# Optimization experiments

Hardware: AMD Instinct MI355X
Metric: run time of the kernel (lower is better)

The kernel has to match this reference:

```python
import jax, jax.numpy as jnp
import numpy as np

N = 100000   # nodes (users+objects merged into one table)
M = 32768    # interactions (edges)
D = 256      # emb_dim == inter_dim
E = 2        # etypes: trusts, rates


def setup_inputs() -> dict:
    key = jax.random.key(0)
    ks = jax.random.split(key, 24)
    s = 1.0 / np.sqrt(D)
    f = lambda k, shp: (jax.random.normal(k, shp, dtype=jnp.float32) * s)
    return {
        "src": jax.random.randint(ks[0], (M,), 0, N),
        "dst": jax.random.randint(ks[1], (M,), 0, N),
        "etype": jax.random.randint(ks[2], (M,), 0, E),
        "dt": jax.random.uniform(ks[3], (M,), dtype=jnp.float32),
        "hid": f(ks[4], (N, D)),
        "cell": f(ks[5], (N, D)),
        # per-etype relation MLPs (source side and target side), layer==1 -> Lin-ReLU-Lin
        "W1s": f(ks[6], (E, D, D)), "b1s": f(ks[7], (E, D)),
        "W2s": f(ks[8], (E, D, D)), "b2s": f(ks[9], (E, D)),
        "W1g": f(ks[10], (E, D, D)), "b1g": f(ks[11], (E, D)),
        "W2g": f(ks[12], (E, D, D)), "b2g": f(ks[13], (E, D)),
        # attention combine (p, q, linear_s, linear_g)
        "p_w": f(ks[14], (D,)), "p_b": jnp.zeros((), jnp.float32),
        "q_w": f(ks[15], (D,)), "q_b": jnp.zeros((), jnp.float32),
        "Ws_w": f(ks[16], (D, D)), "Ws_b": f(ks[17], (D,)),
        "Wg_w": f(ks[18], (D, D)), "Wg_b": f(ks[19], (D,)),
        # time-aware LSTM cell (TLSTMCell(inter_dim=D, emb_dim=D))
        "Wx": f(ks[20], (D, 4 * D)), "Wh": f(ks[21], (D, 4 * D)),
        "b_lstm": jnp.zeros((4 * D,), jnp.float32),
        # final score head
        "w_out": f(ks[22], (D,)), "b_out": jnp.zeros((), jnp.float32),
        "decay_w": jnp.float32(0.1),
    }


def _rel_mlp(x, W1, b1, W2, b2, onehot):
    # x: [M,D]; W1,W2: [E,D,D]; dispatch through per-etype MLP, select by etype.
    h = jax.nn.relu(jnp.einsum('md,edk->emk', x, W1) + b1[:, None, :])   # [E,M,D]
    y = jnp.einsum('emd,edk->emk', h, W2) + b2[:, None, :]               # [E,M,D]
    return jnp.einsum('emd,me->md', y, onehot)                            # [M,D]


def reference(src, dst, etype, dt, hid, cell,
              W1s, b1s, W2s, b2s, W1g, b1g, W2g, b2g,
              p_w, p_b, q_w, q_b, Ws_w, Ws_b, Wg_w, Wg_b,
              Wx, Wh, b_lstm, w_out, b_out, decay_w):
    onehot = jax.nn.one_hot(etype, E, dtype=hid.dtype)  # [M,E]
    h_s = hid[src]   # [M,D] source hidden
    h_g = hid[dst]   # [M,D] target hidden
    c_g = cell[dst]  # [M,D] target cell

    # relation-specific MLPs (RelationNN)
    msg_s = _rel_mlp(h_s, W1s, b1s, W2s, b2s, onehot)
    msg_g = _rel_mlp(h_g, W1g, b1g, W2g, b2g, onehot)

    # attention-gated interaction combine (p/q + linear_s/linear_g)
    a = jax.nn.sigmoid(msg_s @ p_w + p_b + msg_g @ q_w + q_b)[:, None]  # [M,1]
    x = a * (msg_s @ Ws_w.T + Ws_b) + (1.0 - a) * (msg_g @ Wg_w.T + Wg_b)

    # time decay of target cell state (Decay, exp method)
    c_dec = c_g * jnp.exp(-jnp.abs(decay_w) * dt)[:, None]

    # TLSTM cell update for target node
    gates = x @ Wx + h_g @ Wh + b_lstm                                    # [M,4D]
    i_g, f_g, g_g, o_g = jnp.split(gates, 4, axis=-1)
    c_new = jax.nn.sigmoid(f_g) * c_dec + jax.nn.sigmoid(i_g) * jnp.tanh(g_g)
    h_new = jax.nn.sigmoid(o_g) * jnp.tanh(c_new)

    # edge score head (linear -> sigmoid)
    score = jax.nn.sigmoid(h_new @ w_out + b_out)                         # [M]
    return score, h_new, c_new
```

## Files before the change

kernel.cpp:

```cpp
#include <hip/hip_runtime.h>


#define M_EDGES 32768
#define S_TOP   32896
#define TROWS   64
#define GRID_MEGA (S_TOP / TROWS)

typedef __bf16 bf16_t;
typedef __bf16 bf16x8 __attribute__((ext_vector_type(8)));
typedef float  f32x4  __attribute__((ext_vector_type(4)));

#define OFF_W1ST 0
#define OFF_W2ST 131072
#define OFF_W1GT 262144
#define OFF_W2GT 393216
#define OFF_WST  524288
#define OFF_WGT  589824
#define OFF_WXT  655360
#define OFF_WHT  917504
#define WBUF_ELEMS 1179648

__device__ __forceinline__ float sigm_f(float x) { return 1.f / (1.f + __expf(-x)); }
__device__ __forceinline__ float tanh_f(float x) {
  x = fminf(fmaxf(x, -15.f), 15.f);
  float e = __expf(2.f * x);
  return (e - 1.f) / (e + 1.f);
}

__global__ __launch_bounds__(256)
void k_init(const float* __restrict__ W1s, const float* __restrict__ W2s,
            const float* __restrict__ W1g, const float* __restrict__ W2g,
            const float* __restrict__ Wsw, const float* __restrict__ Wgw,
            const float* __restrict__ Wx,  const float* __restrict__ Wh,
            bf16_t* __restrict__ wbuf, int* __restrict__ eid,
            int* __restrict__ srcn, int* __restrict__ dstn,
            float* __restrict__ dts, int* __restrict__ cnt)
{
  const int b = blockIdx.x, tid = threadIdx.x;
  if (b < 256) {
    const float* src; bf16_t* dst; int C_in, n0, k0;
    if (b < 128) {
      const int grp = b >> 5, e = (b >> 4) & 1, t16 = b & 15;
      const float* bases[4] = {W1s, W2s, W1g, W2g};
      src = bases[grp] + e * 65536;
      dst = wbuf + grp * 131072 + e * 65536;
      C_in = 256; n0 = (t16 >> 2) * 64; k0 = (t16 & 3) * 64;
    } else {
      const int b2 = b - 128, mat = b2 >> 6, t64 = b2 & 63;
      src = mat ? Wh : Wx;
      dst = wbuf + OFF_WXT + mat * 262144;
      C_in = 1024; n0 = (t64 >> 2) * 64; k0 = (t64 & 3) * 64;
    }
    __shared__ float tile[64][65];
    const int r = tid >> 2, cg = (tid & 3) * 16;
#pragma unroll
    for (int j = 0; j < 4; ++j) {
      float4 v = *(const float4*)(src + (k0 + r) * C_in + n0 + cg + 4 * j);
      tile[r][cg + 4 * j + 0] = v.x;
      tile[r][cg + 4 * j + 1] = v.y;
      tile[r][cg + 4 * j + 2] = v.z;
      tile[r][cg + 4 * j + 3] = v.w;
    }
    __syncthreads();
    const int c2 = tid >> 2, rg = (tid & 3) * 16;
#pragma unroll
    for (int j = 0; j < 16; ++j)
      dst[(n0 + c2) * 256 + k0 + rg + j] = (bf16_t)tile[rg + j][c2];
  } else {
    const int idx0 = (b - 256) * 256 + tid;
    for (int i = idx0; i < 65536; i += 32768) {
      wbuf[OFF_WST + i] = (bf16_t)Wsw[i];
      wbuf[OFF_WGT + i] = (bf16_t)Wgw[i];
    }
    for (int i = idx0; i < S_TOP; i += 32768) {
      eid[i] = -1; srcn[i] = 0; dstn[i] = 0; dts[i] = 0.f;
    }
    if (idx0 < 2) cnt[idx0] = 0;
  }
}

__global__ __launch_bounds__(256)
void k_slots(const int* __restrict__ etype, const int* __restrict__ src,
             const int* __restrict__ dst, const float* __restrict__ dt,
             int* __restrict__ cnt, int* __restrict__ eid, int* __restrict__ srcn,
             int* __restrict__ dstn, float* __restrict__ dts)
{
  const int m = blockIdx.x * 256 + threadIdx.x;
  const int lane = threadIdx.x & 63;
  const int e = etype[m];
  const unsigned long long b0 = __ballot(e == 0);
  const unsigned long long lt = (1ull << lane) - 1;
  const int c0 = __popcll(b0);
  int a0 = 0, a1 = 0;
  if (lane == 0) {
    a0 = atomicAdd(&cnt[0], c0);
    a1 = atomicAdd(&cnt[1], 64 - c0);
  }
  a0 = __shfl(a0, 0);
  a1 = __shfl(a1, 0);
  const int pos = (e == 0) ? (a0 + __popcll(b0 & lt))
                           : (a1 + __popcll(~b0 & lt));
  const int s = (e == 0) ? pos : (S_TOP - 1 - pos);
  eid[s] = m; srcn[s] = src[m]; dstn[s] = dst[m]; dts[s] = dt[m];
}

__global__ __launch_bounds__(256)
void k_gather(const float* __restrict__ hid, const int* __restrict__ srcn,
              const int* __restrict__ dstn, bf16_t* __restrict__ Xs,
              bf16_t* __restrict__ Xg)
{
  const int s = blockIdx.x * 4 + (threadIdx.x >> 6);
  const int c = (threadIdx.x & 63) * 4;
  const int ns = srcn[s], ng = dstn[s];
  float4 vs = *(const float4*)(hid + (size_t)ns * 256 + c);
  float4 vg = *(const float4*)(hid + (size_t)ng * 256 + c);
  union { bf16_t h[4]; unsigned long long u; } pk;
  pk.h[0] = (bf16_t)vs.x; pk.h[1] = (bf16_t)vs.y; pk.h[2] = (bf16_t)vs.z; pk.h[3] = (bf16_t)vs.w;
  *(unsigned long long*)(Xs + s * 256 + c) = pk.u;
  pk.h[0] = (bf16_t)vg.x; pk.h[1] = (bf16_t)vg.y; pk.h[2] = (bf16_t)vg.z; pk.h[3] = (bf16_t)vg.w;
  *(unsigned long long*)(Xg + s * 256 + c) = pk.u;
}

__device__ __forceinline__ bf16x8 gfrag(const bf16_t* b, int row, int k) {
  return *(const bf16x8*)(b + (size_t)row * 256 + k);
}
__device__ __forceinline__ bf16x8 lfrag(const unsigned short* buf, int row, int kbyte) {
  return *(const bf16x8*)((const char*)buf + row * 512 + (kbyte ^ ((row & 7) << 4)));
}
__device__ __forceinline__ void lstore(unsigned short* buf, int row, int colbyte, bf16_t v) {
  *(bf16_t*)((char*)buf + row * 512 + (colbyte ^ ((row & 7) << 4))) = v;
}
__device__ __forceinline__ float lloadf(const unsigned short* buf, int row, int colbyte) {
  return (float)*(const bf16_t*)((const char*)buf + row * 512 + (colbyte ^ ((row & 7) << 4)));
}
__device__ __forceinline__ void zacc(f32x4 (&acc)[4][4]) {
  const f32x4 z = {0.f, 0.f, 0.f, 0.f};
#pragma unroll
  for (int a = 0; a < 4; ++a)
#pragma unroll
    for (int b = 0; b < 4; ++b) acc[a][b] = z;
}
template<bool LDSA>
__device__ __forceinline__ void gacc(f32x4 (&acc)[4][4], const unsigned short* lb,
                                     const bf16_t* gA, int grow0,
                                     const bf16_t* W, int w, int lo, int hi)
{
#pragma unroll
  for (int c = 0; c < 4; ++c)
#pragma unroll
    for (int ks = 0; ks < 2; ++ks) {
      const int k = c * 64 + ks * 32 + hi * 8;
      bf16x8 af[4];
#pragma unroll
      for (int rb = 0; rb < 4; ++rb) {
        if constexpr (LDSA) af[rb] = lfrag(lb, rb * 16 + lo, k * 2);
        else                af[rb] = gfrag(gA, grow0 + rb * 16 + lo, k);
      }
#pragma unroll
      for (int tc = 0; tc < 4; ++tc) {
        bf16x8 bfv = gfrag(W, w * 64 + tc * 16 + lo, k);
#pragma unroll
        for (int rb = 0; rb < 4; ++rb)
          acc[rb][tc] = __builtin_amdgcn_mfma_f32_16x16x32_bf16(af[rb], bfv, acc[rb][tc], 0, 0, 0);
      }
    }
}

__global__ __launch_bounds__(256, 2)
void k_mega(const bf16_t* __restrict__ Xs, const bf16_t* __restrict__ Xg,
            const bf16_t* __restrict__ wbuf,
            const float* __restrict__ b1s, const float* __restrict__ b2s,
            const float* __restrict__ b1g, const float* __restrict__ b2g,
            const float* __restrict__ p_w, const float* __restrict__ p_b,
            const float* __restrict__ q_w, const float* __restrict__ q_b,
            const float* __restrict__ Wsb, const float* __restrict__ Wgb,
            const float* __restrict__ b_lstm, const float* __restrict__ w_out,
            const float* __restrict__ b_out, const float* __restrict__ decay_w,
            const float* __restrict__ cell, const int* __restrict__ cnt,
            const int* __restrict__ eid, const int* __restrict__ dstn,
            const float* __restrict__ dts,
            float* __restrict__ outS, float* __restrict__ outH, float* __restrict__ outC)
{
  const int tid = threadIdx.x;
  const int w = tid >> 6, lane = tid & 63, lo = lane & 15, hi = lane >> 4;
  const int row0 = blockIdx.x * TROWS;
  const int cnt0 = cnt[0], cnt1 = cnt[1];
  const int cnt0r = (cnt0 + TROWS - 1) & ~(TROWS - 1);
  const int v1 = S_TOP - cnt1;
  if (row0 >= cnt0r && row0 + TROWS <= v1) return;
  const int e = (row0 < cnt0r) ? 0 : 1;

  __shared__ unsigned short bufA[TROWS * 256];
  __shared__ unsigned short bufB[TROWS * 256];
  __shared__ float ps[TROWS], qs[TROWS], aa[TROWS], sdot[TROWS], decv[TROWS];
  __shared__ int leid[TROWS], lnd[TROWS];

  if (tid < TROWS) {
    const int r = row0 + tid;
    ps[tid] = 0.f; qs[tid] = 0.f; sdot[tid] = 0.f;
    leid[tid] = eid[r]; lnd[tid] = dstn[r];
    decv[tid] = __expf(-fabsf(decay_w[0]) * dts[r]);
  }

  f32x4 acc[4][4];

  zacc(acc);
  gacc<false>(acc, nullptr, Xs, row0, wbuf + OFF_W1ST + e * 65536, w, lo, hi);
  {
    const float* bias = b1s + e * 256;
#pragma unroll
    for (int tc = 0; tc < 4; ++tc) {
      const int col = w * 64 + tc * 16 + lo;
      const float bs = bias[col];
#pragma unroll
      for (int rb = 0; rb < 4; ++rb)
#pragma unroll
        for (int i = 0; i < 4; ++i)
          lstore(bufA, rb * 16 + hi * 4 + i, col * 2, (bf16_t)fmaxf(acc[rb][tc][i] + bs, 0.f));
    }
  }
  __syncthreads();

  zacc(acc);
  gacc<true>(acc, bufA, nullptr, 0, wbuf + OFF_W2ST + e * 65536, w, lo, hi);
  {
    const float* bias = b2s + e * 256;
    float dp[4][4] = {};
#pragma unroll
    for (int tc = 0; tc < 4; ++tc) {
      const int col = w * 64 + tc * 16 + lo;
      const float bs = bias[col], pw = p_w[col];
#pragma unroll
      for (int rb = 0; rb < 4; ++rb)
#pragma unroll
        for (int i = 0; i < 4; ++i) {
          const float v = acc[rb][tc][i] + bs;
          lstore(bufB, rb * 16 + hi * 4 + i, col * 2, (bf16_t)v);
          dp[rb][i] += v * pw;
        }
    }
#pragma unroll
    for (int rb = 0; rb < 4; ++rb)
#pragma unroll
      for (int i = 0; i < 4; ++i) {
        float d = dp[rb][i];
        d += __shfl_xor(d, 1); d += __shfl_xor(d, 2);
        d += __shfl_xor(d, 4); d += __shfl_xor(d, 8);
        if (lo == 0) atomicAdd(&ps[rb * 16 + hi * 4 + i], d);
      }
  }
  __syncthreads();

  zacc(acc);
  gacc<true>(acc, bufB, nullptr, 0, wbuf + OFF_WST, w, lo, hi);
#pragma unroll
  for (int tc = 0; tc < 4; ++tc) {
    const float bs = Wsb[w * 64 + tc * 16 + lo];
#pragma unroll
    for (int rb = 0; rb < 4; ++rb)
#pragma unroll
      for (int i = 0; i < 4; ++i) acc[rb][tc][i] += bs;
  }
  __syncthreads();
#pragma unroll
  for (int tc = 0; tc < 4; ++tc) {
    const int col = w * 64 + tc * 16 + lo;
#pragma unroll
    for (int rb = 0; rb < 4; ++rb)
#pragma unroll
      for (int i = 0; i < 4; ++i)
        lstore(bufB, rb * 16 + hi * 4 + i, col * 2, (bf16_t)acc[rb][tc][i]);
  }
  __syncthreads();

  zacc(acc);
  gacc<false>(acc, nullptr, Xg, row0, wbuf + OFF_W1GT + e * 65536, w, lo, hi);
  {
    const float* bias = b1g + e * 256;
#pragma unroll
    for (int tc = 0; tc < 4; ++tc) {
      const int col = w * 64 + tc * 16 + lo;
      const float bs = bias[col];
#pragma unroll
      for (int rb = 0; rb < 4; ++rb)
#pragma unroll
        for (int i = 0; i < 4; ++i)
          lstore(bufA, rb * 16 + hi * 4 + i, col * 2, (bf16_t)fmaxf(acc[rb][tc][i] + bs, 0.f));
    }
  }
  __syncthreads();

  zacc(acc);
  gacc<true>(acc, bufA, nullptr, 0, wbuf + OFF_W2GT + e * 65536, w, lo, hi);
  {
    const float* bias = b2g + e * 256;
    float dp[4][4] = {};
#pragma unroll
    for (int tc = 0; tc < 4; ++tc) {
      const int col = w * 64 + tc * 16 + lo;
      const float bs = bias[col], qw = q_w[col];
#pragma unroll
      for (int rb = 0; rb < 4; ++rb)
#pragma unroll
        for (int i = 0; i < 4; ++i) {
          acc[rb][tc][i] += bs;
          dp[rb][i] += acc[rb][tc][i] * qw;
        }
    }
#pragma unroll
    for (int rb = 0; rb < 4; ++rb)
#pragma unroll
      for (int i = 0; i < 4; ++i) {
        float d = dp[rb][i];
        d += __shfl_xor(d, 1); d += __shfl_xor(d, 2);
        d += __shfl_xor(d, 4); d += __shfl_xor(d, 8);
        if (lo == 0) atomicAdd(&qs[rb * 16 + hi * 4 + i], d);
      }
  }
  __syncthreads();
#pragma unroll
  for (int tc = 0; tc < 4; ++tc) {
    const int col = w * 64 + tc * 16 + lo;
#pragma unroll
    for (int rb = 0; rb < 4; ++rb)
#pragma unroll
      for (int i = 0; i < 4; ++i)
        lstore(bufA, rb * 16 + hi * 4 + i, col * 2, (bf16_t)acc[rb][tc][i]);
  }
  __syncthreads();

  if (tid < TROWS) aa[tid] = sigm_f(ps[tid] + qs[tid] + p_b[0] + q_b[0]);
  __syncthreads();

  zacc(acc);
  gacc<true>(acc, bufA, nullptr, 0, wbuf + OFF_WGT, w, lo, hi);
#pragma unroll
  for (int tc = 0; tc < 4; ++tc) {
    const int col = w * 64 + tc * 16 + lo;
    const float bs = Wgb[col];
#pragma unroll
    for (int rb = 0; rb < 4; ++rb)
#pragma unroll
      for (int i = 0; i < 4; ++i) {
        const int ri = rb * 16 + hi * 4 + i;
        const float av = aa[ri];
        const float tv = lloadf(bufB, ri, col * 2);
        acc[rb][tc][i] = av * tv + (1.f - av) * (acc[rb][tc][i] + bs);
      }
  }
  __syncthreads();
#pragma unroll
  for (int tc = 0; tc < 4; ++tc) {
    const int col = w * 64 + tc * 16 + lo;
#pragma unroll
    for (int rb = 0; rb < 4; ++rb)
#pragma unroll
      for (int i = 0; i < 4; ++i)
        lstore(bufA, rb * 16 + hi * 4 + i, col * 2, (bf16_t)acc[rb][tc][i]);
  }
  __syncthreads();

  zacc(acc);
  gacc<true >(acc, bufA, nullptr, 0, wbuf + OFF_WXT + 2 * 65536, w, lo, hi);
  gacc<false>(acc, nullptr, Xg, row0, wbuf + OFF_WHT + 2 * 65536, w, lo, hi);
#pragma unroll
  for (int tc = 0; tc < 4; ++tc) {
    const int col = w * 64 + tc * 16 + lo;
    const float bs = b_lstm[2 * 256 + col];
#pragma unroll
    for (int rb = 0; rb < 4; ++rb)
#pragma unroll
      for (int i = 0; i < 4; ++i)
        lstore(bufB, rb * 16 + hi * 4 + i, col * 2, (bf16_t)tanh_f(acc[rb][tc][i] + bs));
  }
  zacc(acc);
  gacc<true >(acc, bufA, nullptr, 0, wbuf + OFF_WXT + 0 * 65536, w, lo, hi);
  gacc<false>(acc, nullptr, Xg, row0, wbuf + OFF_WHT + 0 * 65536, w, lo, hi);
#pragma unroll
  for (int tc = 0; tc < 4; ++tc) {
    const int col = w * 64 + tc * 16 + lo;
    const float bs = b_lstm[0 * 256 + col];
#pragma unroll
    for (int rb = 0; rb < 4; ++rb)
#pragma unroll
      for (int i = 0; i < 4; ++i) {
        const int ri = rb * 16 + hi * 4 + i;
        const float c1 = lloadf(bufB, ri, col * 2) * sigm_f(acc[rb][tc][i] + bs);
        lstore(bufB, ri, col * 2, (bf16_t)c1);
      }
  }
  zacc(acc);
  gacc<true >(acc, bufA, nullptr, 0, wbuf + OFF_WXT + 1 * 65536, w, lo, hi);
  gacc<false>(acc, nullptr, Xg, row0, wbuf + OFF_WHT + 1 * 65536, w, lo, hi);
#pragma unroll
  for (int tc = 0; tc < 4; ++tc) {
    const int col = w * 64 + tc * 16 + lo;
    const float bs = b_lstm[1 * 256 + col];
#pragma unroll
    for (int rb = 0; rb < 4; ++rb)
#pragma unroll
      for (int i = 0; i < 4; ++i) {
        const int ri = rb * 16 + hi * 4 + i;
        const float cdec = cell[(size_t)lnd[ri] * 256 + col] * decv[ri];
        const float cn = lloadf(bufB, ri, col * 2) + sigm_f(acc[rb][tc][i] + bs) * cdec;
        lstore(bufB, ri, col * 2, (bf16_t)cn);
      }
  }
  zacc(acc);
  gacc<true >(acc, bufA, nullptr, 0, wbuf + OFF_WXT + 3 * 65536, w, lo, hi);
  gacc<false>(acc, nullptr, Xg, row0, wbuf + OFF_WHT + 3 * 65536, w, lo, hi);
  {
    float dp[4][4] = {};
#pragma unroll
    for (int tc = 0; tc < 4; ++tc) {
      const int col = w * 64 + tc * 16 + lo;
      const float bs = b_lstm[3 * 256 + col];
      const float wo = w_out[col];
#pragma unroll
      for (int rb = 0; rb < 4; ++rb)
#pragma unroll
        for (int i = 0; i < 4; ++i) {
          const int ri = rb * 16 + hi * 4 + i;
          const int m = leid[ri];
          const float cn = lloadf(bufB, ri, col * 2);
          const float hn = sigm_f(acc[rb][tc][i] + bs) * tanh_f(cn);
          if (m >= 0) {
            outH[(size_t)m * 256 + col] = hn;
            outC[(size_t)m * 256 + col] = cn;
          }
          dp[rb][i] += hn * wo;
        }
    }
#pragma unroll
    for (int rb = 0; rb < 4; ++rb)
#pragma unroll
      for (int i = 0; i < 4; ++i) {
        float d = dp[rb][i];
        d += __shfl_xor(d, 1); d += __shfl_xor(d, 2);
        d += __shfl_xor(d, 4); d += __shfl_xor(d, 8);
        if (lo == 0) atomicAdd(&sdot[rb * 16 + hi * 4 + i], d);
      }
  }
  __syncthreads();
  if (tid < TROWS) {
    const int m = leid[tid];
    if (m >= 0) outS[m] = sigm_f(sdot[tid] + b_out[0]);
  }
}

extern "C" void kernel_launch(void* const* d_in, const int* in_sizes, int n_in,
                              void* d_out, int out_size, void* d_ws, size_t ws_size,
                              hipStream_t stream)
{
  const int*   src     = (const int*)d_in[0];
  const int*   dst     = (const int*)d_in[1];
  const int*   etype   = (const int*)d_in[2];
  const float* dt      = (const float*)d_in[3];
  const float* hid     = (const float*)d_in[4];
  const float* cell    = (const float*)d_in[5];
  const float* W1s     = (const float*)d_in[6];
  const float* b1s     = (const float*)d_in[7];
  const float* W2s     = (const float*)d_in[8];
  const float* b2s     = (const float*)d_in[9];
  const float* W1g     = (const float*)d_in[10];
  const float* b1g     = (const float*)d_in[11];
  const float* W2g     = (const float*)d_in[12];
  const float* b2g     = (const float*)d_in[13];
  const float* p_w     = (const float*)d_in[14];
  const float* p_b     = (const float*)d_in[15];
  const float* q_w     = (const float*)d_in[16];
  const float* q_b     = (const float*)d_in[17];
  const float* Ws_w    = (const float*)d_in[18];
  const float* Ws_b    = (const float*)d_in[19];
  const float* Wg_w    = (const float*)d_in[20];
  const float* Wg_b    = (const float*)d_in[21];
  const float* Wx      = (const float*)d_in[22];
  const float* Wh      = (const float*)d_in[23];
  const float* b_lstm  = (const float*)d_in[24];
  const float* w_out   = (const float*)d_in[25];
  const float* b_out   = (const float*)d_in[26];
  const float* decay_w = (const float*)d_in[27];
  (void)in_sizes; (void)n_in; (void)out_size; (void)ws_size;

  char* p = (char*)d_ws;
  auto alloc = [&](size_t bytes) { char* r = p; p += (bytes + 255) & ~(size_t)255; return r; };
  const size_t SB = (size_t)S_TOP * 256 * sizeof(bf16_t);
  bf16_t* wbuf = (bf16_t*)alloc(WBUF_ELEMS * sizeof(bf16_t));
  bf16_t* Xs   = (bf16_t*)alloc(SB);
  bf16_t* Xg   = (bf16_t*)alloc(SB);
  int*    eid  = (int*)alloc(S_TOP * 4);
  int*    srcn = (int*)alloc(S_TOP * 4);
  int*    dstn = (int*)alloc(S_TOP * 4);
  float*  dts  = (float*)alloc(S_TOP * 4);
  int*    cnt  = (int*)alloc(256);

  float* outS = (float*)d_out;
  float* outH = outS + M_EDGES;
  float* outC = outH + (size_t)M_EDGES * 256;

  k_init<<<384, 256, 0, stream>>>(W1s, W2s, W1g, W2g, Ws_w, Wg_w, Wx, Wh,
                                  wbuf, eid, srcn, dstn, dts, cnt);
  k_slots<<<M_EDGES / 256, 256, 0, stream>>>(etype, src, dst, dt, cnt, eid, srcn, dstn, dts);
  k_gather<<<S_TOP / 4, 256, 0, stream>>>(hid, srcn, dstn, Xs, Xg);
  k_mega<<<GRID_MEGA, 256, 0, stream>>>(Xs, Xg, wbuf,
      b1s, b2s, b1g, b2g, p_w, p_b, q_w, q_b, Ws_b, Wg_b,
      b_lstm, w_out, b_out, decay_w, cell, cnt, eid, dstn, dts,
      outS, outH, outC);
}
```

Baseline: 699.0 us.

## Pre-swizzle weights and gathered activations into MFMA fragment order

Weights and gathered hidden rows are now written in a fragment-major layout matching the 16x16x32 MFMA operand pattern, so each lane's bf16x8 load in the GEMM loop is contiguous across the wavefront. Before, every fragment load was a strided row access. The aim is to cut uncoalesced global traffic in the mega kernel. The prep and gather kernels take on more complex index math, and the gather now uses 8 rows per block.

```diff
diff --git a/kernel.cpp b/kernel.cpp
--- a/kernel.cpp
+++ b/kernel.cpp
@@ -25,6 +25,10 @@
   x = fminf(fmaxf(x, -15.f), 15.f);
   float e = __expf(2.f * x);
   return (e - 1.f) / (e + 1.f);
+}
+
+__device__ __forceinline__ int bfrag_off(int n, int k) {
+  return ((n >> 4) * 8 + (k >> 5)) * 512 + ((((k >> 3) & 3) * 16 + (n & 15)) * 8) + (k & 7);
 }
 
 __global__ __launch_bounds__(256)
@@ -38,18 +42,20 @@
 {
   const int b = blockIdx.x, tid = threadIdx.x;
   if (b < 256) {
-    const float* src; bf16_t* dst; int C_in, n0, k0;
+    const float* src; bf16_t* fbase; int C_in, n0, k0, nbase;
     if (b < 128) {
       const int grp = b >> 5, e = (b >> 4) & 1, t16 = b & 15;
       const float* bases[4] = {W1s, W2s, W1g, W2g};
       src = bases[grp] + e * 65536;
-      dst = wbuf + grp * 131072 + e * 65536;
-      C_in = 256; n0 = (t16 >> 2) * 64; k0 = (t16 & 3) * 64;
+      fbase = wbuf + grp * 131072 + e * 65536;
+      C_in = 256; n0 = (t16 >> 2) * 64; k0 = (t16 & 3) * 64; nbase = n0;
     } else {
       const int b2 = b - 128, mat = b2 >> 6, t64 = b2 & 63;
       src = mat ? Wh : Wx;
-      dst = wbuf + OFF_WXT + mat * 262144;
       C_in = 1024; n0 = (t64 >> 2) * 64; k0 = (t64 & 3) * 64;
+      const int gate = n0 >> 8;
+      fbase = wbuf + OFF_WXT + mat * 262144 + gate * 65536;
+      nbase = n0 & 255;
     }
     __shared__ float tile[64][65];
     const int r = tid >> 2, cg = (tid & 3) * 16;
@@ -62,20 +68,35 @@
       tile[r][cg + 4 * j + 3] = v.w;
     }
     __syncthreads();
-    const int c2 = tid >> 2, rg = (tid & 3) * 16;
-#pragma unroll
-    for (int j = 0; j < 16; ++j)
-      dst[(n0 + c2) * 256 + k0 + rg + j] = (bf16_t)tile[rg + j][c2];
+    const int n_local = tid >> 2;
+#pragma unroll
+    for (int gp = 0; gp < 2; ++gp) {
+      const int g = (tid & 3) * 2 + gp;
+      bf16x8 v;
+#pragma unroll
+      for (int jj = 0; jj < 8; ++jj) v[jj] = (bf16_t)tile[g * 8 + jj][n_local];
+      const int n = nbase + n_local, k = k0 + g * 8;
+      *(bf16x8*)(fbase + bfrag_off(n, k)) = v;
+    }
   } else {
-    const int idx0 = (b - 256) * 256 + tid;
-    for (int i = idx0; i < 65536; i += 32768) {
-      wbuf[OFF_WST + i] = (bf16_t)Wsw[i];
-      wbuf[OFF_WGT + i] = (bf16_t)Wgw[i];
-    }
-    for (int i = idx0; i < S_TOP; i += 32768) {
+    const int flat = (b - 256) * 256 + tid;
+    if (flat < 16384) {
+      const int matsel = flat >> 13;
+      const int gi = flat & 8191;
+      const float* srcw = matsel ? Wgw : Wsw;
+      bf16_t* fb = wbuf + (matsel ? OFF_WGT : OFF_WST);
+      const int n = gi >> 5, kg = gi & 31;
+      float4 v0 = *(const float4*)(srcw + n * 256 + kg * 8);
+      float4 v1 = *(const float4*)(srcw + n * 256 + kg * 8 + 4);
+      bf16x8 v;
+      v[0] = (bf16_t)v0.x; v[1] = (bf16_t)v0.y; v[2] = (bf16_t)v0.z; v[3] = (bf16_t)v0.w;
+      v[4] = (bf16_t)v1.x; v[5] = (bf16_t)v1.y; v[6] = (bf16_t)v1.z; v[7] = (bf16_t)v1.w;
+      *(bf16x8*)(fb + bfrag_off(n, kg * 8)) = v;
+    }
+    for (int i = flat; i < S_TOP; i += 32768) {
       eid[i] = -1; srcn[i] = 0; dstn[i] = 0; dts[i] = 0.f;
     }
-    if (idx0 < 2) cnt[idx0] = 0;
+    if (flat < 2) cnt[flat] = 0;
   }
 }
 
@@ -109,21 +130,24 @@
               const int* __restrict__ dstn, bf16_t* __restrict__ Xs,
               bf16_t* __restrict__ Xg)
 {
-  const int s = blockIdx.x * 4 + (threadIdx.x >> 6);
-  const int c = (threadIdx.x & 63) * 4;
+  const int s = blockIdx.x * 8 + (threadIdx.x >> 5);
+  const int kg = threadIdx.x & 31;
   const int ns = srcn[s], ng = dstn[s];
-  float4 vs = *(const float4*)(hid + (size_t)ns * 256 + c);
-  float4 vg = *(const float4*)(hid + (size_t)ng * 256 + c);
-  union { bf16_t h[4]; unsigned long long u; } pk;
-  pk.h[0] = (bf16_t)vs.x; pk.h[1] = (bf16_t)vs.y; pk.h[2] = (bf16_t)vs.z; pk.h[3] = (bf16_t)vs.w;
-  *(unsigned long long*)(Xs + s * 256 + c) = pk.u;
-  pk.h[0] = (bf16_t)vg.x; pk.h[1] = (bf16_t)vg.y; pk.h[2] = (bf16_t)vg.z; pk.h[3] = (bf16_t)vg.w;
-  *(unsigned long long*)(Xg + s * 256 + c) = pk.u;
-}
-
-__device__ __forceinline__ bf16x8 gfrag(const bf16_t* b, int row, int k) {
-  return *(const bf16x8*)(b + (size_t)row * 256 + k);
-}
+  const int t = s >> 6, r = s & 63;
+  const int off = ((t * 4 + (r >> 4)) * 8 + (kg >> 2)) * 512 + (((kg & 3) * 16 + (r & 15)) * 8);
+  float4 a0 = *(const float4*)(hid + (size_t)ns * 256 + kg * 8);
+  float4 a1 = *(const float4*)(hid + (size_t)ns * 256 + kg * 8 + 4);
+  bf16x8 v;
+  v[0] = (bf16_t)a0.x; v[1] = (bf16_t)a0.y; v[2] = (bf16_t)a0.z; v[3] = (bf16_t)a0.w;
+  v[4] = (bf16_t)a1.x; v[5] = (bf16_t)a1.y; v[6] = (bf16_t)a1.z; v[7] = (bf16_t)a1.w;
+  *(bf16x8*)(Xs + off) = v;
+  float4 g0 = *(const float4*)(hid + (size_t)ng * 256 + kg * 8);
+  float4 g1 = *(const float4*)(hid + (size_t)ng * 256 + kg * 8 + 4);
+  v[0] = (bf16_t)g0.x; v[1] = (bf16_t)g0.y; v[2] = (bf16_t)g0.z; v[3] = (bf16_t)g0.w;
+  v[4] = (bf16_t)g1.x; v[5] = (bf16_t)g1.y; v[6] = (bf16_t)g1.z; v[7] = (bf16_t)g1.w;
+  *(bf16x8*)(Xg + off) = v;
+}
+
 __device__ __forceinline__ bf16x8 lfrag(const unsigned short* buf, int row, int kbyte) {
   return *(const bf16x8*)((const char*)buf + row * 512 + (kbyte ^ ((row & 7) << 4)));
 }
@@ -142,23 +166,23 @@
 }
 template<bool LDSA>
 __device__ __forceinline__ void gacc(f32x4 (&acc)[4][4], const unsigned short* lb,
-                                     const bf16_t* gA, int grow0,
-                                     const bf16_t* W, int w, int lo, int hi)
+                                     const bf16_t* gAt, const bf16_t* Wf,
+                                     int w, int lane, int lo, int hi)
 {
 #pragma unroll
   for (int c = 0; c < 4; ++c)
 #pragma unroll
     for (int ks = 0; ks < 2; ++ks) {
-      const int k = c * 64 + ks * 32 + hi * 8;
+      const int kb = c * 2 + ks;
       bf16x8 af[4];
 #pragma unroll
       for (int rb = 0; rb < 4; ++rb) {
-        if constexpr (LDSA) af[rb] = lfrag(lb, rb * 16 + lo, k * 2);
-        else                af[rb] = gfrag(gA, grow0 + rb * 16 + lo, k);
+        if constexpr (LDSA) af[rb] = lfrag(lb, rb * 16 + lo, (c * 64 + ks * 32 + hi * 8) * 2);
+        else                af[rb] = *(const bf16x8*)(gAt + (rb * 8 + kb) * 512 + lane * 8);
       }
 #pragma unroll
       for (int tc = 0; tc < 4; ++tc) {
-        bf16x8 bfv = gfrag(W, w * 64 + tc * 16 + lo, k);
+        bf16x8 bfv = *(const bf16x8*)(Wf + ((w * 4 + tc) * 8 + kb) * 512 + lane * 8);
 #pragma unroll
         for (int rb = 0; rb < 4; ++rb)
           acc[rb][tc] = __builtin_amdgcn_mfma_f32_16x16x32_bf16(af[rb], bfv, acc[rb][tc], 0, 0, 0);
@@ -190,6 +214,9 @@
   if (row0 >= cnt0r && row0 + TROWS <= v1) return;
   const int e = (row0 < cnt0r) ? 0 : 1;
 
+  const bf16_t* XsT = Xs + (row0 >> 6) * 16384;
+  const bf16_t* XgT = Xg + (row0 >> 6) * 16384;
+
   __shared__ unsigned short bufA[TROWS * 256];
   __shared__ unsigned short bufB[TROWS * 256];
   __shared__ float ps[TROWS], qs[TROWS], aa[TROWS], sdot[TROWS], decv[TROWS];
@@ -205,7 +232,7 @@
   f32x4 acc[4][4];
 
   zacc(acc);
-  gacc<false>(acc, nullptr, Xs, row0, wbuf + OFF_W1ST + e * 65536, w, lo, hi);
+  gacc<false>(acc, nullptr, XsT, wbuf + OFF_W1ST + e * 65536, w, lane, lo, hi);
   {
     const float* bias = b1s + e * 256;
 #pragma unroll
@@ -222,7 +249,7 @@
   __syncthreads();
 
   zacc(acc);
-  gacc<true>(acc, bufA, nullptr, 0, wbuf + OFF_W2ST + e * 65536, w, lo, hi);
+  gacc<true>(acc, bufA, nullptr, wbuf + OFF_W2ST + e * 65536, w, lane, lo, hi);
   {
     const float* bias = b2s + e * 256;
     float dp[4][4] = {};
@@ -252,7 +279,7 @@
   __syncthreads();
 
   zacc(acc);
-  gacc<true>(acc, bufB, nullptr, 0, wbuf + OFF_WST, w, lo, hi);
+  gacc<true>(acc, bufB, nullptr, wbuf + OFF_WST, w, lane, lo, hi);
 #pragma unroll
   for (int tc = 0; tc < 4; ++tc) {
     const float bs = Wsb[w * 64 + tc * 16 + lo];
@@ -274,7 +301,7 @@
   __syncthreads();
 
   zacc(acc);
-  gacc<false>(acc, nullptr, Xg, row0, wbuf + OFF_W1GT + e * 65536, w, lo, hi);
+  gacc<false>(acc, nullptr, XgT, wbuf + OFF_W1GT + e * 65536, w, lane, lo, hi);
   {
     const float* bias = b1g + e * 256;
 #pragma unroll
@@ -291,7 +318,7 @@
   __syncthreads();
 
   zacc(acc);
-  gacc<true>(acc, bufA, nullptr, 0, wbuf + OFF_W2GT + e * 65536, w, lo, hi);
+  gacc<true>(acc, bufA, nullptr, wbuf + OFF_W2GT + e * 65536, w, lane, lo, hi);
   {
     const float* bias = b2g + e * 256;
     float dp[4][4] = {};
@@ -333,7 +360,7 @@
   __syncthreads();
 
   zacc(acc);
-  gacc<true>(acc, bufA, nullptr, 0, wbuf + OFF_WGT, w, lo, hi);
+  gacc<true>(acc, bufA, nullptr, wbuf + OFF_WGT, w, lane, lo, hi);
 #pragma unroll
   for (int tc = 0; tc < 4; ++tc) {
     const int col = w * 64 + tc * 16 + lo;
@@ -361,8 +388,8 @@
   __syncthreads();
 
   zacc(acc);
-  gacc<true >(acc, bufA, nullptr, 0, wbuf + OFF_WXT + 2 * 65536, w, lo, hi);
-  gacc<false>(acc, nullptr, Xg, row0, wbuf + OFF_WHT + 2 * 65536, w, lo, hi);
+  gacc<true >(acc, bufA, nullptr, wbuf + OFF_WXT + 2 * 65536, w, lane, lo, hi);
+  gacc<false>(acc, nullptr, XgT, wbuf + OFF_WHT + 2 * 65536, w, lane, lo, hi);
 #pragma unroll
   for (int tc = 0; tc < 4; ++tc) {
     const int col = w * 64 + tc * 16 + lo;
@@ -374,8 +401,8 @@
         lstore(bufB, rb * 16 + hi * 4 + i, col * 2, (bf16_t)tanh_f(acc[rb][tc][i] + bs));
   }
   zacc(acc);
-  gacc<true >(acc, bufA, nullptr, 0, wbuf + OFF_WXT + 0 * 65536, w, lo, hi);
-  gacc<false>(acc, nullptr, Xg, row0, wbuf + OFF_WHT + 0 * 65536, w, lo, hi);
+  gacc<true >(acc, bufA, nullptr, wbuf + OFF_WXT + 0 * 65536, w, lane, lo, hi);
+  gacc<false>(acc, nullptr, XgT, wbuf + OFF_WHT + 0 * 65536, w, lane, lo, hi);
 #pragma unroll
   for (int tc = 0; tc < 4; ++tc) {
     const int col = w * 64 + tc * 16 + lo;
@@ -390,8 +417,8 @@
       }
   }
   zacc(acc);
-  gacc<true >(acc, bufA, nullptr, 0, wbuf + OFF_WXT + 1 * 65536, w, lo, hi);
-  gacc<false>(acc, nullptr, Xg, row0, wbuf + OFF_WHT + 1 * 65536, w, lo, hi);
+  gacc<true >(acc, bufA, nullptr, wbuf + OFF_WXT + 1 * 65536, w, lane, lo, hi);
+  gacc<false>(acc, nullptr, XgT, wbuf + OFF_WHT + 1 * 65536, w, lane, lo, hi);
 #pragma unroll
   for (int tc = 0; tc < 4; ++tc) {
     const int col = w * 64 + tc * 16 + lo;
@@ -407,8 +434,8 @@
       }
   }
   zacc(acc);
-  gacc<true >(acc, bufA, nullptr, 0, wbuf + OFF_WXT + 3 * 65536, w, lo, hi);
-  gacc<false>(acc, nullptr, Xg, row0, wbuf + OFF_WHT + 3 * 65536, w, lo, hi);
+  gacc<true >(acc, bufA, nullptr, wbuf + OFF_WXT + 3 * 65536, w, lane, lo, hi);
+  gacc<false>(acc, nullptr, XgT, wbuf + OFF_WHT + 3 * 65536, w, lane, lo, hi);
   {
     float dp[4][4] = {};
 #pragma unroll
@@ -501,7 +528,7 @@
   k_init<<<384, 256, 0, stream>>>(W1s, W2s, W1g, W2g, Ws_w, Wg_w, Wx, Wh,
                                   wbuf, eid, srcn, dstn, dts, cnt);
   k_slots<<<M_EDGES / 256, 256, 0, stream>>>(etype, src, dst, dt, cnt, eid, srcn, dstn, dts);
-  k_gather<<<S_TOP / 4, 256, 0, stream>>>(hid, srcn, dstn, Xs, Xg);
+  k_gather<<<S_TOP / 8, 256, 0, stream>>>(hid, srcn, dstn, Xs, Xg);
   k_mega<<<GRID_MEGA, 256, 0, stream>>>(Xs, Xg, wbuf,
       b1s, b2s, b1g, b2g, p_w, p_b, q_w, q_b, Ws_b, Wg_b,
       b_lstm, w_out, b_out, decay_w, cell, cnt, eid, dstn, dts,
```

Measured after the change: 687.4 us. Within noise of the previous version (-1.7%).
